# Kernel optimization log

Hardware: AMD Instinct MI355X
Metric: run time of the kernel (lower is better)

Reference implementation:

```python
import jax, jax.numpy as jnp
import numpy as np

B, H, IN, OUT = 8192, 1024, 4, 4


def setup_inputs() -> dict:
    key = jax.random.key(0)
    ks = jax.random.split(key, 16)
    s = 1.0 / np.sqrt(H)

    def p(k, shape):
        return jax.random.uniform(k, shape, jnp.float32, -s, s)

    return {
        "context": jax.random.normal(ks[0], (B, H), jnp.float32),
        "wc": p(ks[1], (H // 2, H)),
        "bc": p(ks[2], (H // 2,)),
        "gru1_wi": p(ks[3], (3 * H, H // 2)),
        "gru1_wh": p(ks[4], (3 * H, H)),
        "gru1_bi": p(ks[5], (3 * H,)),
        "gru1_bh": p(ks[6], (3 * H,)),
        "gru2_wi": p(ks[7], (3 * H, H // 2)),
        "gru2_wh": p(ks[8], (3 * H, H)),
        "gru2_bi": p(ks[9], (3 * H,)),
        "gru2_bh": p(ks[10], (3 * H,)),
        "fc_in_w": p(ks[11], (IN, H)),
        "fc_in_b": p(ks[12], (IN,)),
        "fc_out_w": p(ks[13], (OUT, H)),
        "fc_out_b": p(ks[14], (OUT,)),
        "future_length": 30,
        "past_length": 60,
    }


def _gru_unroll(ec, h0, wi, wh, bi, bh, length):
    """Run a PyTorch-semantics GRUCell `length` steps with constant input ec.

    Returns all hidden states stacked: [T, B, H].
    """
    # Input-side gates are constant across steps (input is always ec).
    gi = ec @ wi.T + bi                     # [B, 3H]
    i_r, i_z, i_n = jnp.split(gi, 3, axis=-1)

    def step(h, _):
        gh = h @ wh.T + bh                  # [B, 3H]
        h_r, h_z, h_n = jnp.split(gh, 3, axis=-1)
        r = jax.nn.sigmoid(i_r + h_r)
        z = jax.nn.sigmoid(i_z + h_z)
        n = jnp.tanh(i_n + r * h_n)
        h_new = (1.0 - z) * n + z * h
        return h_new, h_new

    _, hs = jax.lax.scan(step, h0, None, length=length)
    return hs  # [T, B, H]


def reference(context, wc, bc,
              gru1_wi, gru1_wh, gru1_bi, gru1_bh,
              gru2_wi, gru2_wh, gru2_bi, gru2_bh,
              fc_in_w, fc_in_b, fc_out_w, fc_out_b,
              future_length, past_length):
    # encoded_context = relu(context_encoder(context))
    ec = jax.nn.relu(context @ wc.T + bc)   # [B, H/2]

    # Training-mode past-reconstruction branch (decoder1 + fc_in).
    hs1 = _gru_unroll(ec, context, gru1_wi, gru1_wh, gru1_bi, gru1_bh, past_length)
    decoded_inputs = jnp.einsum('tbh,ih->bti', hs1, fc_in_w) + fc_in_b  # [B, T_past, IN]

    # Future-prediction branch (decoder2 + relu + fc_out).
    hs2 = _gru_unroll(ec, context, gru2_wi, gru2_wh, gru2_bi, gru2_bh, future_length)
    outputs = jnp.einsum('tbh,oh->bto', jax.nn.relu(hs2), fc_out_w) + fc_out_b  # [B, T_fut, OUT]

    return (decoded_inputs, outputs)
```

## Files before the change

kernel.cpp:

```cpp
#include <hip/hip_runtime.h>
#include <math.h>

typedef __bf16 bf16;
typedef __bf16 bf16x8 __attribute__((ext_vector_type(8)));
typedef float f32x4 __attribute__((ext_vector_type(4)));

#define B_DIM 8192
#define H_DIM 1024
#define T_PAST 60
#define T_FUT 30

static __device__ __forceinline__ void gld_lds16(const void* g, void* l) {
  __builtin_amdgcn_global_load_lds(
      (const __attribute__((address_space(1))) void*)g,
      (__attribute__((address_space(3))) void*)l, 16, 0, 0);
}

static __device__ __forceinline__ float sigm(float x) {
  return 1.f / (1.f + __expf(-x));
}
static __device__ __forceinline__ float tanh_fast(float x) {
  float xc = fminf(fmaxf(x, -10.f), 10.f);
  float e = __expf(2.f * xc);
  return (e - 1.f) / (e + 1.f);
}

__global__ void detect_dtype(const unsigned int* __restrict__ words,
                             int* __restrict__ is_bf16) {
  const int lane = threadIdx.x;
  int cnt = 0;
  for (int i = 0; i < 64; i++) {
    const unsigned int w = words[lane + i * 64];
    const int e = (w >> 7) & 0xFF;
    cnt += (e >= 100 && e <= 135) ? 1 : 0;
  }
  for (int off = 32; off > 0; off >>= 1) cnt += __shfl_down(cnt, off);
  if (lane == 0) *is_bf16 = (cnt >= 2048) ? 1 : 0;
}

struct ConvDesc { const void* src; bf16* dst; int n; };
struct ConvPack { ConvDesc d[15]; };

__global__ __launch_bounds__(256) void convert_all(ConvPack p,
                                                   const int* __restrict__ flag,
                                                   float* __restrict__ h0a,
                                                   float* __restrict__ h0b) {
  const int ti = blockIdx.y;
  const ConvDesc d = p.d[ti];
  const int bf = *flag;
  const long stride = (long)gridDim.x * 256 * 8;
  for (long base = ((long)blockIdx.x * 256 + threadIdx.x) * 8; base < d.n;
       base += stride) {
    if (base + 8 <= d.n) {
      float f[8];
      if (bf) {
        const uint4 v = *(const uint4*)((const char*)d.src + base * 2);
        *(uint4*)((char*)d.dst + base * 2) = v;
        if (ti == 0 && h0a) {
          const bf16* bv = (const bf16*)&v;
#pragma unroll
          for (int e = 0; e < 8; e++) f[e] = (float)bv[e];
        }
      } else {
        const float* s = (const float*)d.src + base;
        const float4 v0 = *(const float4*)s;
        const float4 v1 = *(const float4*)(s + 4);
        f[0] = v0.x; f[1] = v0.y; f[2] = v0.z; f[3] = v0.w;
        f[4] = v1.x; f[5] = v1.y; f[6] = v1.z; f[7] = v1.w;
        bf16 o[8];
#pragma unroll
        for (int e = 0; e < 8; e++) o[e] = (bf16)f[e];
        *(uint4*)((char*)d.dst + base * 2) = *(const uint4*)o;
      }
      if (ti == 0 && h0a) {
#pragma unroll
        for (int e = 0; e < 8; e++) { h0a[base + e] = f[e]; h0b[base + e] = f[e]; }
      }
    } else {
      for (long e = base; e < d.n; e++) {
        const float f = bf ? (float)((const bf16*)d.src)[e]
                           : ((const float*)d.src)[e];
        d.dst[e] = (bf16)f;
        if (ti == 0 && h0a) { h0a[e] = f; h0b[e] = f; }
      }
    }
  }
}

template <bool RELU, bool GI_BIAS>
__global__ __launch_bounds__(256, 2) void gemm_bt(
    const bf16* __restrict__ A, const bf16* __restrict__ Bm,
    const bf16* __restrict__ bias1, const bf16* __restrict__ bias2,
    bf16* __restrict__ C, int K, int N)
{
  __shared__ __attribute__((aligned(16))) bf16 As[128 * 32];
  __shared__ __attribute__((aligned(16))) bf16 Bs[128 * 32];
  const int tid = threadIdx.x;
  const int wave = tid >> 6, lane = tid & 63;
  const int quad = lane >> 4, l16 = lane & 15;
  const int m0 = blockIdx.x * 128, n0 = blockIdx.y * 128;
  const int wm = (wave & 1) * 64, wn = (wave >> 1) * 64;
  f32x4 acc[4][4] = {};
  for (int k0 = 0; k0 < K; k0 += 32) {
#pragma unroll
    for (int rr = 0; rr < 2; rr++) {
      const int c = rr * 256 + tid;
      const int cg = (c & 3) ^ ((c >> 3) & 3);
      gld_lds16(A + (size_t)(m0 + (c >> 2)) * K + (k0 + cg * 8),
                As + (size_t)(rr * 256 + wave * 64) * 8);
      gld_lds16(Bm + (size_t)(n0 + (c >> 2)) * K + (k0 + cg * 8),
                Bs + (size_t)(rr * 256 + wave * 64) * 8);
    }
    __syncthreads();
    bf16x8 af[4], bv[4];
#pragma unroll
    for (int t = 0; t < 4; t++) {
      const int ra = wm + t * 16 + l16;
      const int rb = wn + t * 16 + l16;
      af[t] = *(const bf16x8*)(As + (ra * 32 + (quad ^ ((ra >> 1) & 3)) * 8));
      bv[t] = *(const bf16x8*)(Bs + (rb * 32 + (quad ^ ((rb >> 1) & 3)) * 8));
    }
#pragma unroll
    for (int tm = 0; tm < 4; tm++)
#pragma unroll
      for (int tn = 0; tn < 4; tn++)
        acc[tm][tn] = __builtin_amdgcn_mfma_f32_16x16x32_bf16(af[tm], bv[tn], acc[tm][tn], 0, 0, 0);
    __syncthreads();
  }
#pragma unroll
  for (int tn = 0; tn < 4; tn++) {
    const int col = n0 + wn + tn * 16 + l16;
    float bias = (float)bias1[col];
    if (GI_BIAS) {
      if (col < 2 * H_DIM) bias += (float)bias2[col];
    }
#pragma unroll
    for (int tm = 0; tm < 4; tm++) {
#pragma unroll
      for (int r = 0; r < 4; r++) {
        const int row = m0 + wm + tm * 16 + quad * 4 + r;
        float v = acc[tm][tn][r] + bias;
        if (RELU) v = fmaxf(v, 0.f);
        C[(size_t)row * N + col] = (bf16)v;
      }
    }
  }
}

struct GruArgs {
  const bf16* h_in16; const float* h_in32;
  bf16* h_out16; float* h_out32;
  const bf16* gi;
  const bf16* wh;
  const bf16* bh;
  const bf16* fcw;
  float* proj;
  int projT, t, relu;
};

__global__ __launch_bounds__(256, 4) void gru_step(GruArgs g1, GruArgs g2)
{
  const GruArgs G = (blockIdx.z == 0) ? g1 : g2;
  __shared__ __attribute__((aligned(16))) bf16 As[64 * 32];
  __shared__ __attribute__((aligned(16))) bf16 Bs[192 * 32];
  __shared__ __attribute__((aligned(16))) bf16 Gs[64 * 192];
  const int tid = threadIdx.x;
  const int wave = tid >> 6, lane = tid & 63;
  const int quad = lane >> 4, l16 = lane & 15;
  const int m0 = blockIdx.x * 64;
  const int j0 = blockIdx.y * 64;
  f32x4 acc[12] = {};
  for (int k0 = 0; k0 < H_DIM; k0 += 32) {
    {
      const int c = tid;
      const int cg = (c & 3) ^ ((c >> 3) & 3);
      gld_lds16(G.h_in16 + (size_t)(m0 + (c >> 2)) * H_DIM + (k0 + cg * 8),
                As + (size_t)(wave * 64) * 8);
    }
#pragma unroll
    for (int rr = 0; rr < 3; rr++) {
      const int c = rr * 256 + tid;
      const int p = c >> 2;
      const int cg = (c & 3) ^ ((c >> 3) & 3);
      const int grow = (p >> 6) * H_DIM + j0 + (p & 63);
      gld_lds16(G.wh + (size_t)grow * H_DIM + (k0 + cg * 8),
                Bs + (size_t)(rr * 256 + wave * 64) * 8);
    }
    __syncthreads();
    const int ra = wave * 16 + l16;
    bf16x8 af = *(const bf16x8*)(As + (ra * 32 + (quad ^ ((ra >> 1) & 3)) * 8));
#pragma unroll
    for (int tn = 0; tn < 12; tn++) {
      const int rb = tn * 16 + l16;
      bf16x8 bv = *(const bf16x8*)(Bs + (rb * 32 + (quad ^ ((rb >> 1) & 3)) * 8));
      acc[tn] = __builtin_amdgcn_mfma_f32_16x16x32_bf16(af, bv, acc[tn], 0, 0, 0);
    }
    __syncthreads();
  }

#pragma unroll
  for (int i = 0; i < 6; i++) {
    const int L = i * 256 + tid;
    const int row = L / 24, c = L % 24;
    gld_lds16(G.gi + (size_t)(m0 + row) * (3 * H_DIM) +
                  ((c >> 3) * H_DIM + j0 + (c & 7) * 8),
              Gs + (size_t)(i * 256 + wave * 64) * 8);
  }
  __syncthreads();

  float pp[4][4];
#pragma unroll
  for (int r = 0; r < 4; r++)
#pragma unroll
    for (int i = 0; i < 4; i++) pp[r][i] = 0.f;

#pragma unroll
  for (int tj = 0; tj < 4; tj++) {
    const int jj = tj * 16 + l16;
    const int j = j0 + jj;
    const float bhn = (float)G.bh[2 * H_DIM + j];
    float fw[4];
#pragma unroll
    for (int i = 0; i < 4; i++) fw[i] = (float)G.fcw[i * H_DIM + j];
#pragma unroll
    for (int r = 0; r < 4; r++) {
      const int lrow = wave * 16 + quad * 4 + r;
      const int row = m0 + lrow;
      const float gr = (float)Gs[lrow * 192 + jj];
      const float gz = (float)Gs[lrow * 192 + 64 + jj];
      const float gn = (float)Gs[lrow * 192 + 128 + jj];
      const float hr = acc[tj][r];
      const float hz = acc[tj + 4][r];
      const float hn = acc[tj + 8][r];
      const float rg = sigm(gr + hr);
      const float zg = sigm(gz + hz);
      const float ng = tanh_fast(gn + rg * (hn + bhn));
      const size_t hidx = (size_t)row * H_DIM + j;
      const float hold = G.h_in32 ? G.h_in32[hidx] : (float)G.h_in16[hidx];
      const float hnew = (1.f - zg) * ng + zg * hold;
      if (G.h_out32) G.h_out32[hidx] = hnew;
      G.h_out16[hidx] = (bf16)hnew;
      const float act = G.relu ? fmaxf(hnew, 0.f) : hnew;
#pragma unroll
      for (int i = 0; i < 4; i++) pp[r][i] += fw[i] * act;
    }
  }
#pragma unroll
  for (int r = 0; r < 4; r++)
#pragma unroll
    for (int i = 0; i < 4; i++) {
      float v = pp[r][i];
      v += __shfl_xor(v, 1);
      v += __shfl_xor(v, 2);
      v += __shfl_xor(v, 4);
      v += __shfl_xor(v, 8);
      if (l16 == 0) {
        const int row = m0 + wave * 16 + quad * 4 + r;
        atomicAdd(&G.proj[((size_t)row * G.projT + G.t) * 4 + i], v);
      }
    }
}

__global__ __launch_bounds__(256) void finalize(const float* __restrict__ p1,
                                                const float* __restrict__ p2,
                                                const bf16* __restrict__ fib,
                                                const bf16* __restrict__ fob,
                                                const int* __restrict__ flag,
                                                void* __restrict__ out, int n) {
  const int idx = blockIdx.x * 256 + threadIdx.x;
  if (idx >= n) return;
  const int R1 = B_DIM * T_PAST * 4;
  float v;
  if (idx < R1) {
    v = p1[idx] + (float)fib[idx & 3];
  } else {
    const int k = idx - R1;
    v = p2[k] + (float)fob[k & 3];
  }
  if (*flag) ((bf16*)out)[idx] = (bf16)v;
  else       ((float*)out)[idx] = v;
}

extern "C" void kernel_launch(void* const* d_in, const int* in_sizes, int n_in,
                              void* d_out, int out_size, void* d_ws, size_t ws_size,
                              hipStream_t stream)
{
  (void)n_in;
  char* w = (char*)d_ws;
  auto alloc = [&](size_t bytes) -> void* {
    void* p = (void*)w;
    w += (bytes + 255) & ~(size_t)255;
    return p;
  };
  int* flag = (int*)alloc(256);

  bf16* canon[15];
  for (int i = 0; i < 15; i++) canon[i] = (bf16*)alloc((size_t)in_sizes[i] * 2);
  const bf16* ctx  = canon[0];
  const bf16* wc   = canon[1];
  const bf16* bc   = canon[2];
  const bf16* g1wi = canon[3];
  const bf16* g1wh = canon[4];
  const bf16* g1bi = canon[5];
  const bf16* g1bh = canon[6];
  const bf16* g2wi = canon[7];
  const bf16* g2wh = canon[8];
  const bf16* g2bi = canon[9];
  const bf16* g2bh = canon[10];
  const bf16* fiw  = canon[11];
  const bf16* fib  = canon[12];
  const bf16* fow  = canon[13];
  const bf16* fob  = canon[14];

  bf16* ec   = (bf16*)alloc((size_t)B_DIM * 512 * 2);
  bf16* gi1  = (bf16*)alloc((size_t)B_DIM * 3 * H_DIM * 2);
  bf16* gi2  = (bf16*)alloc((size_t)B_DIM * 3 * H_DIM * 2);
  bf16* h116[2] = {(bf16*)alloc((size_t)B_DIM * H_DIM * 2), (bf16*)alloc((size_t)B_DIM * H_DIM * 2)};
  bf16* h216[2] = {(bf16*)alloc((size_t)B_DIM * H_DIM * 2), (bf16*)alloc((size_t)B_DIM * H_DIM * 2)};
  float* proj1 = (float*)alloc((size_t)B_DIM * T_PAST * 4 * 4);
  float* proj2 = (float*)alloc((size_t)B_DIM * T_FUT * 4 * 4);
  float* h132[2] = {nullptr, nullptr};
  float* h232[2] = {nullptr, nullptr};
  const size_t used = (size_t)(w - (char*)d_ws);
  const size_t fp32_need = (size_t)4 * B_DIM * H_DIM * 4 + 4096;
  const bool fp32h = (ws_size > used) && ((ws_size - used) >= fp32_need);
  if (fp32h) {
    h132[0] = (float*)alloc((size_t)B_DIM * H_DIM * 4);
    h132[1] = (float*)alloc((size_t)B_DIM * H_DIM * 4);
    h232[0] = (float*)alloc((size_t)B_DIM * H_DIM * 4);
    h232[1] = (float*)alloc((size_t)B_DIM * H_DIM * 4);
  }

  detect_dtype<<<1, 64, 0, stream>>>((const unsigned int*)d_in[0], flag);

  hipMemsetAsync(proj1, 0,
                 ((size_t)B_DIM * T_PAST * 4 + (size_t)B_DIM * T_FUT * 4) * 4, stream);

  ConvPack cp;
  for (int i = 0; i < 15; i++) { cp.d[i].src = d_in[i]; cp.d[i].dst = canon[i]; cp.d[i].n = in_sizes[i]; }
  convert_all<<<dim3(4096, 15), 256, 0, stream>>>(cp, flag,
      fp32h ? h132[0] : nullptr, fp32h ? h232[0] : nullptr);

  gemm_bt<true, false><<<dim3(64, 4), 256, 0, stream>>>(ctx, wc, bc, nullptr, ec, H_DIM, 512);
  gemm_bt<false, true><<<dim3(64, 24), 256, 0, stream>>>(ec, g1wi, g1bi, g1bh, gi1, 512, 3 * H_DIM);
  gemm_bt<false, true><<<dim3(64, 24), 256, 0, stream>>>(ec, g2wi, g2bi, g2bh, gi2, 512, 3 * H_DIM);

  for (int t = 0; t < T_PAST; t++) {
    const int si = t & 1, so = (t + 1) & 1;
    GruArgs a1;
    a1.h_in16 = (t == 0) ? ctx : h116[si];
    a1.h_in32 = fp32h ? h132[si] : nullptr;
    a1.h_out16 = h116[so];
    a1.h_out32 = fp32h ? h132[so] : nullptr;
    a1.gi = gi1; a1.wh = g1wh; a1.bh = g1bh; a1.fcw = fiw;
    a1.proj = proj1; a1.projT = T_PAST; a1.t = t; a1.relu = 0;
    if (t < T_FUT) {
      GruArgs a2;
      a2.h_in16 = (t == 0) ? ctx : h216[si];
      a2.h_in32 = fp32h ? h232[si] : nullptr;
      a2.h_out16 = h216[so];
      a2.h_out32 = fp32h ? h232[so] : nullptr;
      a2.gi = gi2; a2.wh = g2wh; a2.bh = g2bh; a2.fcw = fow;
      a2.proj = proj2; a2.projT = T_FUT; a2.t = t; a2.relu = 1;
      gru_step<<<dim3(128, 16, 2), 256, 0, stream>>>(a1, a2);
    } else {
      gru_step<<<dim3(128, 16, 1), 256, 0, stream>>>(a1, a1);
    }
  }

  finalize<<<dim3((out_size + 255) / 256), 256, 0, stream>>>(
      proj1, proj2, fib, fob, flag, d_out, out_size);
}
```

Baseline: 9.114 ms.

## Use 32x32x16 MFMA with 2x2 wave tiling and direct global A-operand loads

The recurrent GEMM in the GRU step kernel moves from 16x16x32 MFMA with per-wave 16-row strips to 32x32x16 MFMA, with each wave owning a 32-row by 32-column tile across the three gates. The h operand is now read straight from global memory into registers instead of being staged through shared memory, so only the weight tile goes through LDS. Shared-memory use for A is dropped, and the gi prefetch now overlaps the K loop. The risk is that uncoalesced, per-lane 16-byte global A loads with no reuse across waves raise memory latency, and the epilogue now does more shuffle reductions.

```diff
diff --git a/kernel.cpp b/kernel.cpp
--- a/kernel.cpp
+++ b/kernel.cpp
@@ -4,6 +4,7 @@
 typedef __bf16 bf16;
 typedef __bf16 bf16x8 __attribute__((ext_vector_type(8)));
 typedef float f32x4 __attribute__((ext_vector_type(4)));
+typedef float f32x16 __attribute__((ext_vector_type(16)));
 
 #define B_DIM 8192
 #define H_DIM 1024
@@ -161,42 +162,15 @@
 __global__ __launch_bounds__(256, 4) void gru_step(GruArgs g1, GruArgs g2)
 {
   const GruArgs G = (blockIdx.z == 0) ? g1 : g2;
-  __shared__ __attribute__((aligned(16))) bf16 As[64 * 32];
-  __shared__ __attribute__((aligned(16))) bf16 Bs[192 * 32];
+  __shared__ __attribute__((aligned(16))) bf16 Bs[4 * 192 * 8];
   __shared__ __attribute__((aligned(16))) bf16 Gs[64 * 192];
   const int tid = threadIdx.x;
   const int wave = tid >> 6, lane = tid & 63;
-  const int quad = lane >> 4, l16 = lane & 15;
+  const int half = lane >> 5, l32 = lane & 31;
   const int m0 = blockIdx.x * 64;
   const int j0 = blockIdx.y * 64;
-  f32x4 acc[12] = {};
-  for (int k0 = 0; k0 < H_DIM; k0 += 32) {
-    {
-      const int c = tid;
-      const int cg = (c & 3) ^ ((c >> 3) & 3);
-      gld_lds16(G.h_in16 + (size_t)(m0 + (c >> 2)) * H_DIM + (k0 + cg * 8),
-                As + (size_t)(wave * 64) * 8);
-    }
-#pragma unroll
-    for (int rr = 0; rr < 3; rr++) {
-      const int c = rr * 256 + tid;
-      const int p = c >> 2;
-      const int cg = (c & 3) ^ ((c >> 3) & 3);
-      const int grow = (p >> 6) * H_DIM + j0 + (p & 63);
-      gld_lds16(G.wh + (size_t)grow * H_DIM + (k0 + cg * 8),
-                Bs + (size_t)(rr * 256 + wave * 64) * 8);
-    }
-    __syncthreads();
-    const int ra = wave * 16 + l16;
-    bf16x8 af = *(const bf16x8*)(As + (ra * 32 + (quad ^ ((ra >> 1) & 3)) * 8));
-#pragma unroll
-    for (int tn = 0; tn < 12; tn++) {
-      const int rb = tn * 16 + l16;
-      bf16x8 bv = *(const bf16x8*)(Bs + (rb * 32 + (quad ^ ((rb >> 1) & 3)) * 8));
-      acc[tn] = __builtin_amdgcn_mfma_f32_16x16x32_bf16(af, bv, acc[tn], 0, 0, 0);
-    }
-    __syncthreads();
-  }
+  const int Rw = (wave & 1) * 32;
+  const int jw = (wave >> 1) * 32;
 
 #pragma unroll
   for (int i = 0; i < 6; i++) {
@@ -206,59 +180,79 @@
                   ((c >> 3) * H_DIM + j0 + (c & 7) * 8),
               Gs + (size_t)(i * 256 + wave * 64) * 8);
   }
-  __syncthreads();
-
-  float pp[4][4];
-#pragma unroll
-  for (int r = 0; r < 4; r++)
-#pragma unroll
-    for (int i = 0; i < 4; i++) pp[r][i] = 0.f;
-
-#pragma unroll
-  for (int tj = 0; tj < 4; tj++) {
-    const int jj = tj * 16 + l16;
-    const int j = j0 + jj;
-    const float bhn = (float)G.bh[2 * H_DIM + j];
-    float fw[4];
-#pragma unroll
-    for (int i = 0; i < 4; i++) fw[i] = (float)G.fcw[i * H_DIM + j];
+
+  const bf16* Ap = G.h_in16 + (size_t)(m0 + Rw + l32) * H_DIM + half * 8;
+  const bf16* Bp = Bs + ((size_t)half * 192 + jw + l32) * 8;
+
+  f32x16 acc[3] = {};
+  for (int kt = 0; kt < 32; kt++) {
+    __syncthreads();
+#pragma unroll
+    for (int rr = 0; rr < 3; rr++) {
+      gld_lds16(G.wh + (size_t)(rr * H_DIM + j0 + lane) * H_DIM + (kt * 32 + wave * 8),
+                Bs + ((size_t)wave * 192 + rr * 64) * 8);
+    }
+    __syncthreads();
+    const bf16x8 a0 = *(const bf16x8*)(Ap + kt * 32);
+    const bf16x8 a1 = *(const bf16x8*)(Ap + kt * 32 + 16);
+#pragma unroll
+    for (int g = 0; g < 3; g++) {
+      const bf16x8 b0 = *(const bf16x8*)(Bp + g * 512);
+      const bf16x8 b1 = *(const bf16x8*)(Bp + 3072 + g * 512);
+      acc[g] = __builtin_amdgcn_mfma_f32_32x32x16_bf16(a0, b0, acc[g], 0, 0, 0);
+      acc[g] = __builtin_amdgcn_mfma_f32_32x32x16_bf16(a1, b1, acc[g], 0, 0, 0);
+    }
+  }
+
+  const int jcol = jw + l32;
+  const int jglob = j0 + jcol;
+  const float bhn = (float)G.bh[2 * H_DIM + jglob];
+  float fw[4];
+#pragma unroll
+  for (int i = 0; i < 4; i++) fw[i] = (float)G.fcw[i * H_DIM + jglob];
+
+#pragma unroll
+  for (int Q = 0; Q < 4; Q++) {
+    float pp[4][4];
 #pragma unroll
     for (int r = 0; r < 4; r++) {
-      const int lrow = wave * 16 + quad * 4 + r;
+      const int reg = Q * 4 + r;
+      const int lrow = Rw + r + 8 * Q + 4 * half;
       const int row = m0 + lrow;
-      const float gr = (float)Gs[lrow * 192 + jj];
-      const float gz = (float)Gs[lrow * 192 + 64 + jj];
-      const float gn = (float)Gs[lrow * 192 + 128 + jj];
-      const float hr = acc[tj][r];
-      const float hz = acc[tj + 4][r];
-      const float hn = acc[tj + 8][r];
+      const float gr = (float)Gs[lrow * 192 + jcol];
+      const float gz = (float)Gs[lrow * 192 + 64 + jcol];
+      const float gn = (float)Gs[lrow * 192 + 128 + jcol];
+      const float hr = acc[0][reg];
+      const float hz = acc[1][reg];
+      const float hn = acc[2][reg];
       const float rg = sigm(gr + hr);
       const float zg = sigm(gz + hz);
       const float ng = tanh_fast(gn + rg * (hn + bhn));
-      const size_t hidx = (size_t)row * H_DIM + j;
+      const size_t hidx = (size_t)row * H_DIM + jglob;
       const float hold = G.h_in32 ? G.h_in32[hidx] : (float)G.h_in16[hidx];
       const float hnew = (1.f - zg) * ng + zg * hold;
       if (G.h_out32) G.h_out32[hidx] = hnew;
       G.h_out16[hidx] = (bf16)hnew;
       const float act = G.relu ? fmaxf(hnew, 0.f) : hnew;
 #pragma unroll
-      for (int i = 0; i < 4; i++) pp[r][i] += fw[i] * act;
-    }
-  }
-#pragma unroll
-  for (int r = 0; r < 4; r++)
-#pragma unroll
-    for (int i = 0; i < 4; i++) {
-      float v = pp[r][i];
-      v += __shfl_xor(v, 1);
-      v += __shfl_xor(v, 2);
-      v += __shfl_xor(v, 4);
-      v += __shfl_xor(v, 8);
-      if (l16 == 0) {
-        const int row = m0 + wave * 16 + quad * 4 + r;
-        atomicAdd(&G.proj[((size_t)row * G.projT + G.t) * 4 + i], v);
-      }
-    }
+      for (int i = 0; i < 4; i++) pp[r][i] = fw[i] * act;
+    }
+#pragma unroll
+    for (int r = 0; r < 4; r++)
+#pragma unroll
+      for (int i = 0; i < 4; i++) {
+        float v = pp[r][i];
+        v += __shfl_xor(v, 1);
+        v += __shfl_xor(v, 2);
+        v += __shfl_xor(v, 4);
+        v += __shfl_xor(v, 8);
+        v += __shfl_xor(v, 16);
+        if (l32 == 0) {
+          const int row = m0 + Rw + r + 8 * Q + 4 * half;
+          atomicAdd(&G.proj[((size_t)row * G.projT + G.t) * 4 + i], v);
+        }
+      }
+  }
 }
 
 __global__ __launch_bounds__(256) void finalize(const float* __restrict__ p1,
```

Result: slower. 18.63 ms (+104.5%).

## Repartition GRU step waves by hidden-unit columns across all block rows

Applied to the files above, without the earlier changes.

Each wave now owns 16 hidden units (all three gates) across all 64 rows of the block, instead of 16 rows across all 192 gate columns. This cuts LDS fragment reads per k-step from 13 to 7 while keeping 12 MFMAs. The gi tile prefetch is also issued before the main loop so it overlaps the GEMM. In exchange, the fc projection reduction is no longer summed across column tiles in registers, so the number of shuffles and atomicAdds per block rises about fourfold.

```diff
diff --git a/kernel.cpp b/kernel.cpp
--- a/kernel.cpp
+++ b/kernel.cpp
@@ -169,34 +169,6 @@
   const int quad = lane >> 4, l16 = lane & 15;
   const int m0 = blockIdx.x * 64;
   const int j0 = blockIdx.y * 64;
-  f32x4 acc[12] = {};
-  for (int k0 = 0; k0 < H_DIM; k0 += 32) {
-    {
-      const int c = tid;
-      const int cg = (c & 3) ^ ((c >> 3) & 3);
-      gld_lds16(G.h_in16 + (size_t)(m0 + (c >> 2)) * H_DIM + (k0 + cg * 8),
-                As + (size_t)(wave * 64) * 8);
-    }
-#pragma unroll
-    for (int rr = 0; rr < 3; rr++) {
-      const int c = rr * 256 + tid;
-      const int p = c >> 2;
-      const int cg = (c & 3) ^ ((c >> 3) & 3);
-      const int grow = (p >> 6) * H_DIM + j0 + (p & 63);
-      gld_lds16(G.wh + (size_t)grow * H_DIM + (k0 + cg * 8),
-                Bs + (size_t)(rr * 256 + wave * 64) * 8);
-    }
-    __syncthreads();
-    const int ra = wave * 16 + l16;
-    bf16x8 af = *(const bf16x8*)(As + (ra * 32 + (quad ^ ((ra >> 1) & 3)) * 8));
-#pragma unroll
-    for (int tn = 0; tn < 12; tn++) {
-      const int rb = tn * 16 + l16;
-      bf16x8 bv = *(const bf16x8*)(Bs + (rb * 32 + (quad ^ ((rb >> 1) & 3)) * 8));
-      acc[tn] = __builtin_amdgcn_mfma_f32_16x16x32_bf16(af, bv, acc[tn], 0, 0, 0);
-    }
-    __syncthreads();
-  }
 
 #pragma unroll
   for (int i = 0; i < 6; i++) {
@@ -206,59 +178,87 @@
                   ((c >> 3) * H_DIM + j0 + (c & 7) * 8),
               Gs + (size_t)(i * 256 + wave * 64) * 8);
   }
-  __syncthreads();
-
-  float pp[4][4];
-#pragma unroll
-  for (int r = 0; r < 4; r++)
-#pragma unroll
-    for (int i = 0; i < 4; i++) pp[r][i] = 0.f;
-
-#pragma unroll
-  for (int tj = 0; tj < 4; tj++) {
-    const int jj = tj * 16 + l16;
-    const int j = j0 + jj;
-    const float bhn = (float)G.bh[2 * H_DIM + j];
-    float fw[4];
-#pragma unroll
-    for (int i = 0; i < 4; i++) fw[i] = (float)G.fcw[i * H_DIM + j];
+
+  f32x4 acc[4][3] = {};
+  for (int kt = 0; kt < 32; kt++) {
+    const int k0 = kt * 32;
+    {
+      const int c = tid;
+      const int cg = (c & 3) ^ ((c >> 3) & 3);
+      gld_lds16(G.h_in16 + (size_t)(m0 + (c >> 2)) * H_DIM + (k0 + cg * 8),
+                As + (size_t)(wave * 64) * 8);
+    }
+#pragma unroll
+    for (int i = 0; i < 3; i++) {
+      const int c = i * 256 + tid;
+      const int q = c >> 2;
+      const int jblock = q / 48, rem = q % 48;
+      const int g = rem >> 4, jl = rem & 15;
+      const int cg = (c & 3) ^ ((c >> 3) & 3);
+      gld_lds16(G.wh + (size_t)(g * H_DIM + j0 + jblock * 16 + jl) * H_DIM + (k0 + cg * 8),
+                Bs + (size_t)(i * 256 + wave * 64) * 8);
+    }
+    __syncthreads();
+    bf16x8 bf[3];
+#pragma unroll
+    for (int g = 0; g < 3; g++) {
+      const int q = wave * 48 + g * 16 + l16;
+      bf[g] = *(const bf16x8*)(Bs + (q * 32 + (quad ^ ((q >> 1) & 3)) * 8));
+    }
+#pragma unroll
+    for (int mf = 0; mf < 4; mf++) {
+      const int ra = mf * 16 + l16;
+      const bf16x8 af = *(const bf16x8*)(As + (ra * 32 + (quad ^ ((ra >> 1) & 3)) * 8));
+#pragma unroll
+      for (int g = 0; g < 3; g++)
+        acc[mf][g] = __builtin_amdgcn_mfma_f32_16x16x32_bf16(af, bf[g], acc[mf][g], 0, 0, 0);
+    }
+    __syncthreads();
+  }
+
+  const int jl = wave * 16 + l16;
+  const int jglob = j0 + jl;
+  const float bhn = (float)G.bh[2 * H_DIM + jglob];
+  float fw[4];
+#pragma unroll
+  for (int i = 0; i < 4; i++) fw[i] = (float)G.fcw[i * H_DIM + jglob];
+
+#pragma unroll
+  for (int mf = 0; mf < 4; mf++) {
 #pragma unroll
     for (int r = 0; r < 4; r++) {
-      const int lrow = wave * 16 + quad * 4 + r;
+      const int lrow = mf * 16 + quad * 4 + r;
       const int row = m0 + lrow;
-      const float gr = (float)Gs[lrow * 192 + jj];
-      const float gz = (float)Gs[lrow * 192 + 64 + jj];
-      const float gn = (float)Gs[lrow * 192 + 128 + jj];
-      const float hr = acc[tj][r];
-      const float hz = acc[tj + 4][r];
-      const float hn = acc[tj + 8][r];
+      const float gr = (float)Gs[lrow * 192 + jl];
+      const float gz = (float)Gs[lrow * 192 + 64 + jl];
+      const float gn = (float)Gs[lrow * 192 + 128 + jl];
+      const float hr = acc[mf][0][r];
+      const float hz = acc[mf][1][r];
+      const float hn = acc[mf][2][r];
       const float rg = sigm(gr + hr);
       const float zg = sigm(gz + hz);
       const float ng = tanh_fast(gn + rg * (hn + bhn));
-      const size_t hidx = (size_t)row * H_DIM + j;
+      const size_t hidx = (size_t)row * H_DIM + jglob;
       const float hold = G.h_in32 ? G.h_in32[hidx] : (float)G.h_in16[hidx];
       const float hnew = (1.f - zg) * ng + zg * hold;
       if (G.h_out32) G.h_out32[hidx] = hnew;
       G.h_out16[hidx] = (bf16)hnew;
       const float act = G.relu ? fmaxf(hnew, 0.f) : hnew;
-#pragma unroll
-      for (int i = 0; i < 4; i++) pp[r][i] += fw[i] * act;
-    }
-  }
-#pragma unroll
-  for (int r = 0; r < 4; r++)
-#pragma unroll
-    for (int i = 0; i < 4; i++) {
-      float v = pp[r][i];
-      v += __shfl_xor(v, 1);
-      v += __shfl_xor(v, 2);
-      v += __shfl_xor(v, 4);
-      v += __shfl_xor(v, 8);
-      if (l16 == 0) {
-        const int row = m0 + wave * 16 + quad * 4 + r;
-        atomicAdd(&G.proj[((size_t)row * G.projT + G.t) * 4 + i], v);
-      }
-    }
+      float pp[4];
+#pragma unroll
+      for (int i = 0; i < 4; i++) pp[i] = fw[i] * act;
+#pragma unroll
+      for (int i = 0; i < 4; i++) {
+        float v = pp[i];
+        v += __shfl_xor(v, 1);
+        v += __shfl_xor(v, 2);
+        v += __shfl_xor(v, 4);
+        v += __shfl_xor(v, 8);
+        if (l16 == 0)
+          atomicAdd(&G.proj[((size_t)row * G.projT + G.t) * 4 + i], v);
+      }
+    }
+  }
 }
 
 __global__ __launch_bounds__(256) void finalize(const float* __restrict__ p1,
```

New measurement: 14.97 ms. 64.2% more time.
